# Optimization experiments

Measured on AMD Instinct MI355X. Metric: run time of the kernel, lower is better.

The kernel has to match this reference:

```python
import jax, jax.numpy as jnp
import numpy as np

N_NODES = 50000
N_EDGES = 800000
NODE_DIM = 64
EDGE_DIM = 32
OUT_FEATS = 64


def setup_inputs() -> dict:
    key = jax.random.key(0)
    k1, k2, k3, k4, k5, k6, k7 = jax.random.split(key, 7)
    node_features = jax.random.normal(k1, (N_NODES, NODE_DIM), dtype=jnp.float32)
    edge_features = jax.random.normal(k2, (N_EDGES, EDGE_DIM), dtype=jnp.float32)
    src = jax.random.randint(k3, (N_EDGES,), 0, N_NODES, dtype=jnp.int32)
    dst = jax.random.randint(k4, (N_EDGES,), 0, N_NODES, dtype=jnp.int32)
    in_dim = 2 * NODE_DIM + EDGE_DIM  # concat([e_ft, h_src, h_dst])
    w_group = jax.random.normal(k5, (in_dim,), dtype=jnp.float32) * 0.05
    w_srcattn = jax.random.normal(k6, (NODE_DIM + EDGE_DIM,), dtype=jnp.float32) * 0.05
    w_lin = jax.random.normal(k7, (in_dim, OUT_FEATS), dtype=jnp.float32) * 0.05
    return {"node_features": node_features, "edge_features": edge_features,
            "src": src, "dst": dst,
            "w_group": w_group, "w_srcattn": w_srcattn, "w_lin": w_lin}


def _segment_softmax(scores, seg, num_segments):
    # numerically-stable softmax of per-edge scalar scores within each segment
    m = jax.ops.segment_max(scores, seg, num_segments=num_segments)
    e = jnp.exp(scores - m[seg])
    s = jax.ops.segment_sum(e, seg, num_segments=num_segments)
    return e / s[seg]


def reference(node_features, edge_features, src, dst, w_group, w_srcattn, w_lin):
    h = node_features              # [N, node_dim]
    e_ft = edge_features           # [E, edge_dim]
    h_src = h[src]                 # [E, node_dim]
    h_dst = h[dst]                 # [E, node_dim]

    # --- group_apply_edges(group_by='src'): edge attention over out-edges of each src ---
    z2 = jnp.concatenate([e_ft, h_src, h_dst], axis=1)      # [E, edge_dim + 2*node_dim]
    a = z2 @ w_group                                        # [E]
    gamma = _segment_softmax(a, src, N_NODES)               # softmax over edges sharing src
    e_weighted = gamma[:, None] * e_ft                      # [E, edge_dim]

    # --- gnn_msg: msg = concat([h_src, e_weighted]) ---
    msg = jnp.concatenate([h_src, e_weighted], axis=1)      # [E, node_dim + edge_dim]

    # --- gnn_reduce: attention softmax over mailbox (edges sharing dst), weighted sum ---
    s = msg @ w_srcattn                                     # [E]
    alpha = _segment_softmax(s, dst, N_NODES)
    accum = jax.ops.segment_sum(alpha[:, None] * msg, dst, num_segments=N_NODES)  # [N, node_dim+edge_dim]

    # --- node_update: linear(concat([h, accum])) + relu ---
    h_cat = jnp.concatenate([h, accum], axis=1)             # [N, 2*node_dim + edge_dim]
    out = jax.nn.relu(h_cat @ w_lin)                        # [N, out_feats]
    return out
```

## Files before the change

### kernel.cpp

```cpp
#include <hip/hip_runtime.h>

#define NN 50000
#define NE 800000
#define NHB 3125
#define NTILES 3125

typedef __attribute__((ext_vector_type(8))) short bf16x8;
typedef __attribute__((ext_vector_type(4))) float f32x4;

static __device__ __forceinline__ short f2bf(float f) {
    unsigned int u = __float_as_uint(f);
    u += 0x7FFFu + ((u >> 16) & 1u);
    return (short)(u >> 16);
}

__global__ __launch_bounds__(256) void k_pre(
    const float* __restrict__ h, const int* __restrict__ dst,
    const float* __restrict__ wg, const float* __restrict__ wa,
    int* __restrict__ cnt, int* __restrict__ rank,
    float* __restrict__ p1, float* __restrict__ pd, float* __restrict__ dpf)
{
    int tid = threadIdx.x;
    if (blockIdx.x < NHB) {
        int e = blockIdx.x * 256 + tid;
        if (e < NE) rank[e] = atomicAdd(&cnt[dst[e]], 1);
        return;
    }
    __shared__ float4 ls[16], ld[16], lt[16];
    if (tid < 16)      ls[tid]      = ((const float4*)wg)[8 + tid];
    else if (tid < 32) ld[tid - 16] = ((const float4*)wg)[8 + tid];
    else if (tid < 48) lt[tid - 32] = ((const float4*)wa)[tid - 32];
    __syncthreads();
    int n = (blockIdx.x - NHB) * 16 + (tid >> 4);
    if (n >= NN) return;
    int l16 = tid & 15;
    float4 v = ((const float4*)(h + (size_t)n * 64))[l16];
    float4 w1 = ls[l16], w2 = ld[l16], w3 = lt[l16];
    float s1 = v.x*w1.x + v.y*w1.y + v.z*w1.z + v.w*w1.w;
    float s2 = v.x*w2.x + v.y*w2.y + v.z*w2.z + v.w*w2.w;
    float s3 = v.x*w3.x + v.y*w3.y + v.z*w3.z + v.w*w3.w;
    #pragma unroll
    for (int m = 8; m; m >>= 1) {
        s1 += __shfl_xor(s1, m);
        s2 += __shfl_xor(s2, m);
        s3 += __shfl_xor(s3, m);
    }
    if (l16 == 0) { p1[n] = s1; pd[n] = s2; dpf[2 * n + 1] = s3; }
}

__global__ __launch_bounds__(256) void k_assign(
    const int* __restrict__ cnt, int* __restrict__ off, int* __restrict__ gtotal)
{
    int n = blockIdx.x * 256 + threadIdx.x;
    int lane = threadIdx.x & 63;
    int c = (n < NN) ? cnt[n] : 0;
    int pre = c;
    #pragma unroll
    for (int d = 1; d < 64; d <<= 1) {
        int v = __shfl_up(pre, d);
        if (lane >= d) pre += v;
    }
    int base = 0;
    if (lane == 63) base = atomicAdd(gtotal, pre);
    base = __shfl(base, 63);
    if (n < NN) off[n] = base + pre - c;
}

__global__ __launch_bounds__(256) void k_edge(
    const float* __restrict__ ef, const int* __restrict__ src,
    const int* __restrict__ dst, const int* __restrict__ rank,
    const float* __restrict__ wg, const float* __restrict__ wa,
    const float* __restrict__ p1, const float* __restrict__ pd,
    float* __restrict__ dpf, const int* __restrict__ off,
    int4* __restrict__ recA)
{
    __shared__ float4 lwe[8], lae[8];
    int tid = threadIdx.x;
    if (tid < 8)       lwe[tid]     = ((const float4*)wg)[tid];
    else if (tid < 16) lae[tid - 8] = ((const float4*)wa)[tid - 8 + 16];
    __syncthreads();
    int e = blockIdx.x * 256 + tid;
    if (e >= NE) return;
    int s = src[e], d = dst[e], rk = rank[e];
    const float4* e4 = (const float4*)(ef + (size_t)e * 32);
    float a = 0.f, u = 0.f;
    #pragma unroll
    for (int q = 0; q < 8; ++q) {
        float4 v = e4[q], w = lwe[q], w2 = lae[q];
        a += v.x*w.x  + v.y*w.y  + v.z*w.z  + v.w*w.w;
        u += v.x*w2.x + v.y*w2.y + v.z*w2.z + v.w*w2.w;
    }
    a += p1[s] + pd[d];
    float eav = __expf(a);
    atomicAdd(&dpf[2 * s], eav);
    int pos = off[d] + rk;
    recA[pos] = make_int4(s, e, __float_as_int(eav), __float_as_int(u));
}

__global__ __launch_bounds__(256) void k_reduce(
    const float* __restrict__ h, const float* __restrict__ ef,
    const int* __restrict__ cnt, const int* __restrict__ off,
    const float2* __restrict__ dp, const int4* __restrict__ recA,
    float* __restrict__ accum)
{
    int n = blockIdx.x * 4 + (threadIdx.x >> 6);
    if (n >= NN) return;
    int lane = threadIdx.x & 63;
    bool up = lane >= 32;
    int l5 = lane & 31;
    int deg = cnt[n], base = off[n];
    float acch = 0.f, acce = 0.f, den = 0.f;
    int j = 0;
    for (; j + 4 <= deg; j += 4) {
        int4 r0 = recA[base+j+0], r1 = recA[base+j+1];
        int4 r2 = recA[base+j+2], r3 = recA[base+j+3];
        float2 d0 = dp[r0.x], d1 = dp[r1.x], d2 = dp[r2.x], d3 = dp[r3.x];
        float h0 = h[(size_t)r0.x*64+lane], h1 = h[(size_t)r1.x*64+lane];
        float h2 = h[(size_t)r2.x*64+lane], h3 = h[(size_t)r3.x*64+lane];
        int eA = up ? r1.y : r0.y, eB = up ? r3.y : r2.y;
        float efA = ef[(size_t)eA*32 + l5];
        float efB = ef[(size_t)eB*32 + l5];
        float g0 = __int_as_float(r0.z)/d0.x, g1 = __int_as_float(r1.z)/d1.x;
        float g2 = __int_as_float(r2.z)/d2.x, g3 = __int_as_float(r3.z)/d3.x;
        float s0 = __expf(d0.y + g0*__int_as_float(r0.w));
        float s1 = __expf(d1.y + g1*__int_as_float(r1.w));
        float s2 = __expf(d2.y + g2*__int_as_float(r2.w));
        float s3 = __expf(d3.y + g3*__int_as_float(r3.w));
        den  += s0 + s1 + s2 + s3;
        acch += s0*h0 + s1*h1 + s2*h2 + s3*h3;
        float wA = up ? s1*g1 : s0*g0;
        float wB = up ? s3*g3 : s2*g2;
        acce += wA*efA + wB*efB;
    }
    for (; j < deg; ++j) {
        int4 r = recA[base+j];
        float2 dt = dp[r.x];
        float g = __int_as_float(r.z)/dt.x;
        float s = __expf(dt.y + g*__int_as_float(r.w));
        den += s;
        acch += s * h[(size_t)r.x*64+lane];
        if (!up) acce += s * g * ef[(size_t)r.y*32 + l5];
    }
    acce += __shfl_xor(acce, 32);
    float inv = (deg > 0) ? 1.f/den : 0.f;
    accum[(size_t)n*96 + lane] = acch * inv;
    if (!up) accum[(size_t)n*96 + 64 + lane] = acce * inv;
}

__global__ __launch_bounds__(256) void k_node_update(
    const float* __restrict__ h, const float* __restrict__ accum,
    const float* __restrict__ wl_g, float* __restrict__ out)
{
    int lane = threadIdx.x & 63;
    int col  = lane & 15;
    int quad = lane >> 4;
    int wid  = blockIdx.x * 4 + (threadIdx.x >> 6);
    int nwaves = gridDim.x * 4;

    bf16x8 bfr[5][4];
    #pragma unroll
    for (int kc = 0; kc < 5; ++kc)
        #pragma unroll
        for (int nt = 0; nt < 4; ++nt) {
            #pragma unroll
            for (int j = 0; j < 8; ++j) {
                int k = kc * 32 + quad * 8 + j;
                bfr[kc][nt][j] = f2bf(wl_g[k * 64 + nt * 16 + col]);
            }
        }

    for (int tile = wid; tile < NTILES; tile += nwaves) {
        int n = tile * 16 + col;
        f32x4 acc[4];
        #pragma unroll
        for (int nt = 0; nt < 4; ++nt) acc[nt] = (f32x4){0.f, 0.f, 0.f, 0.f};

        #pragma unroll
        for (int kc = 0; kc < 5; ++kc) {
            int kbase = kc * 32 + quad * 8;
            const float* p = (kbase < 64)
                ? (h     + (size_t)n * 64 + kbase)
                : (accum + (size_t)n * 96 + (kbase - 64));
            float4 va = *(const float4*)p;
            float4 vb = *(const float4*)(p + 4);
            bf16x8 af;
            af[0] = f2bf(va.x); af[1] = f2bf(va.y);
            af[2] = f2bf(va.z); af[3] = f2bf(va.w);
            af[4] = f2bf(vb.x); af[5] = f2bf(vb.y);
            af[6] = f2bf(vb.z); af[7] = f2bf(vb.w);
            #pragma unroll
            for (int nt = 0; nt < 4; ++nt)
                acc[nt] = __builtin_amdgcn_mfma_f32_16x16x32_bf16(
                    af, bfr[kc][nt], acc[nt], 0, 0, 0);
        }

        #pragma unroll
        for (int nt = 0; nt < 4; ++nt) {
            #pragma unroll
            for (int r = 0; r < 4; ++r) {
                int node = tile * 16 + quad * 4 + r;
                out[(size_t)node * 64 + nt * 16 + col] = fmaxf(acc[nt][r], 0.f);
            }
        }
    }
}

extern "C" void kernel_launch(void* const* d_in, const int* in_sizes, int n_in,
                              void* d_out, int out_size, void* d_ws, size_t ws_size,
                              hipStream_t stream)
{
    const float* h   = (const float*)d_in[0];
    const float* ef  = (const float*)d_in[1];
    const int*   src = (const int*)d_in[2];
    const int*   dst = (const int*)d_in[3];
    const float* wg  = (const float*)d_in[4];
    const float* wa  = (const float*)d_in[5];
    const float* wl  = (const float*)d_in[6];
    float* out = (float*)d_out;

    float* ws = (float*)d_ws;
    float*  dpf    = ws;
    int*    cnt    = (int*)(ws + 2 * NN);
    int*    gtotal = (int*)(ws + 3 * NN);
    int*    off    = (int*)(ws + 3 * NN + 16);
    float*  p1     = ws + 4 * NN + 16;
    float*  pd     = ws + 5 * NN + 16;
    int4*   recA   = (int4*)(ws + 6 * NN + 16);
    int*    rank   = (int*)(ws + 6 * NN + 16 + 4 * NE);
    float*  accum  = ws + 6 * NN + 16 + 4 * NE;

    hipMemsetAsync(d_ws, 0, (size_t)(3 * NN + 16) * sizeof(float), stream);

    k_pre<<<2 * NHB, 256, 0, stream>>>(h, dst, wg, wa, cnt, rank, p1, pd, dpf);
    k_assign<<<(NN + 255) / 256, 256, 0, stream>>>(cnt, off, gtotal);
    k_edge<<<NHB, 256, 0, stream>>>(ef, src, dst, rank, wg, wa, p1, pd, dpf,
                                    off, recA);
    k_reduce<<<(NN + 3) / 4, 256, 0, stream>>>(h, ef, cnt, off, (const float2*)dpf,
                                               recA, accum);
    k_node_update<<<256, 256, 0, stream>>>(h, accum, wl, out);
}
```

Before: 334.9 us.

## Pack bf16 node/accum rows, two edges per thread, deeper reduce unroll

Node features are converted to bf16 in the pre-pass and the reduce kernel writes its aggregated results as bf16 into the same 160-wide row buffer. The node-update GEMM can then load MFMA operands directly, with no fp32 loads or per-element conversion, and it runs one tile per wave. The edge and rank kernels handle two edges per thread and write records with nontemporal stores. The reduce loop is unrolled by 8 and uses rcp approximations in place of divides. This trades some accuracy (fast rcp, bf16 rounding of accum, which the old code also did at GEMM time) for less memory traffic and more memory-level parallelism.

```diff
diff --git a/kernel.cpp b/kernel.cpp
--- a/kernel.cpp
+++ b/kernel.cpp
@@ -2,11 +2,14 @@
 
 #define NN 50000
 #define NE 800000
+#define NEB 1563
 #define NHB 3125
 #define NTILES 3125
 
 typedef __attribute__((ext_vector_type(8))) short bf16x8;
+typedef __attribute__((ext_vector_type(4))) short s16x4;
 typedef __attribute__((ext_vector_type(4))) float f32x4;
+typedef __attribute__((ext_vector_type(4))) int   i32x4;
 
 static __device__ __forceinline__ short f2bf(float f) {
     unsigned int u = __float_as_uint(f);
@@ -18,12 +21,21 @@
     const float* __restrict__ h, const int* __restrict__ dst,
     const float* __restrict__ wg, const float* __restrict__ wa,
     int* __restrict__ cnt, int* __restrict__ rank,
-    float* __restrict__ p1, float* __restrict__ pd, float* __restrict__ dpf)
+    float* __restrict__ p1, float* __restrict__ pd, float* __restrict__ dpf,
+    short* __restrict__ hb)
 {
     int tid = threadIdx.x;
-    if (blockIdx.x < NHB) {
-        int e = blockIdx.x * 256 + tid;
-        if (e < NE) rank[e] = atomicAdd(&cnt[dst[e]], 1);
+    if (blockIdx.x < NEB) {
+        int e0 = blockIdx.x * 512 + tid;
+        if (e0 >= NE) return;
+        int e1 = e0 + 256;
+        bool v1 = e1 < NE;
+        int d0 = dst[e0];
+        int d1 = dst[v1 ? e1 : 0];
+        int r0 = atomicAdd(&cnt[d0], 1);
+        int r1 = v1 ? atomicAdd(&cnt[d1], 1) : 0;
+        rank[e0] = r0;
+        if (v1) rank[e1] = r1;
         return;
     }
     __shared__ float4 ls[16], ld[16], lt[16];
@@ -31,10 +43,13 @@
     else if (tid < 32) ld[tid - 16] = ((const float4*)wg)[8 + tid];
     else if (tid < 48) lt[tid - 32] = ((const float4*)wa)[tid - 32];
     __syncthreads();
-    int n = (blockIdx.x - NHB) * 16 + (tid >> 4);
+    int n = (blockIdx.x - NEB) * 16 + (tid >> 4);
     if (n >= NN) return;
     int l16 = tid & 15;
     float4 v = ((const float4*)(h + (size_t)n * 64))[l16];
+    s16x4 hv;
+    hv[0] = f2bf(v.x); hv[1] = f2bf(v.y); hv[2] = f2bf(v.z); hv[3] = f2bf(v.w);
+    *(s16x4*)(hb + (size_t)n * 160 + l16 * 4) = hv;
     float4 w1 = ls[l16], w2 = ld[l16], w3 = lt[l16];
     float s1 = v.x*w1.x + v.y*w1.y + v.z*w1.z + v.w*w1.w;
     float s2 = v.x*w2.x + v.y*w2.y + v.z*w2.z + v.w*w2.w;
@@ -72,36 +87,52 @@
     const float* __restrict__ wg, const float* __restrict__ wa,
     const float* __restrict__ p1, const float* __restrict__ pd,
     float* __restrict__ dpf, const int* __restrict__ off,
-    int4* __restrict__ recA)
+    i32x4* __restrict__ recA)
 {
     __shared__ float4 lwe[8], lae[8];
     int tid = threadIdx.x;
     if (tid < 8)       lwe[tid]     = ((const float4*)wg)[tid];
     else if (tid < 16) lae[tid - 8] = ((const float4*)wa)[tid - 8 + 16];
     __syncthreads();
-    int e = blockIdx.x * 256 + tid;
-    if (e >= NE) return;
-    int s = src[e], d = dst[e], rk = rank[e];
-    const float4* e4 = (const float4*)(ef + (size_t)e * 32);
-    float a = 0.f, u = 0.f;
+    int e0 = blockIdx.x * 512 + tid;
+    if (e0 >= NE) return;
+    int e1 = e0 + 256;
+    bool v1 = e1 < NE;
+    int e1c = v1 ? e1 : 0;
+    int s0 = src[e0], d0 = dst[e0], k0 = rank[e0];
+    int s1 = src[e1c], d1 = dst[e1c], k1 = rank[e1c];
+    float p1a = p1[s0], pda = pd[d0];
+    float p1b = p1[s1], pdb = pd[d1];
+    int o0 = off[d0], o1 = off[d1];
+    const float4* ea = (const float4*)ef + (unsigned)e0 * 8u;
+    const float4* eb = (const float4*)ef + (unsigned)e1c * 8u;
+    float a0 = 0.f, u0 = 0.f, a1 = 0.f, u1 = 0.f;
     #pragma unroll
     for (int q = 0; q < 8; ++q) {
-        float4 v = e4[q], w = lwe[q], w2 = lae[q];
-        a += v.x*w.x  + v.y*w.y  + v.z*w.z  + v.w*w.w;
-        u += v.x*w2.x + v.y*w2.y + v.z*w2.z + v.w*w2.w;
-    }
-    a += p1[s] + pd[d];
-    float eav = __expf(a);
-    atomicAdd(&dpf[2 * s], eav);
-    int pos = off[d] + rk;
-    recA[pos] = make_int4(s, e, __float_as_int(eav), __float_as_int(u));
+        float4 x = ea[q], y = eb[q];
+        float4 w = lwe[q], w2 = lae[q];
+        a0 += x.x*w.x  + x.y*w.y  + x.z*w.z  + x.w*w.w;
+        u0 += x.x*w2.x + x.y*w2.y + x.z*w2.z + x.w*w2.w;
+        a1 += y.x*w.x  + y.y*w.y  + y.z*w.z  + y.w*w.w;
+        u1 += y.x*w2.x + y.y*w2.y + y.z*w2.z + y.w*w2.w;
+    }
+    float ev0 = __expf(a0 + p1a + pda);
+    float ev1 = __expf(a1 + p1b + pdb);
+    atomicAdd(&dpf[2 * s0], ev0);
+    if (v1) atomicAdd(&dpf[2 * s1], ev1);
+    i32x4 rc0 = (i32x4){s0, e0, __float_as_int(ev0), __float_as_int(u0)};
+    __builtin_nontemporal_store(rc0, recA + (o0 + k0));
+    if (v1) {
+        i32x4 rc1 = (i32x4){s1, e1, __float_as_int(ev1), __float_as_int(u1)};
+        __builtin_nontemporal_store(rc1, recA + (o1 + k1));
+    }
 }
 
 __global__ __launch_bounds__(256) void k_reduce(
     const float* __restrict__ h, const float* __restrict__ ef,
     const int* __restrict__ cnt, const int* __restrict__ off,
-    const float2* __restrict__ dp, const int4* __restrict__ recA,
-    float* __restrict__ accum)
+    const float2* __restrict__ dp, const i32x4* __restrict__ recA,
+    short* __restrict__ hb)
 {
     int n = blockIdx.x * 4 + (threadIdx.x >> 6);
     if (n >= NN) return;
@@ -109,53 +140,95 @@
     bool up = lane >= 32;
     int l5 = lane & 31;
     int deg = cnt[n], base = off[n];
+    const i32x4* rp = recA + base;
     float acch = 0.f, acce = 0.f, den = 0.f;
     int j = 0;
-    for (; j + 4 <= deg; j += 4) {
-        int4 r0 = recA[base+j+0], r1 = recA[base+j+1];
-        int4 r2 = recA[base+j+2], r3 = recA[base+j+3];
-        float2 d0 = dp[r0.x], d1 = dp[r1.x], d2 = dp[r2.x], d3 = dp[r3.x];
-        float h0 = h[(size_t)r0.x*64+lane], h1 = h[(size_t)r1.x*64+lane];
-        float h2 = h[(size_t)r2.x*64+lane], h3 = h[(size_t)r3.x*64+lane];
-        int eA = up ? r1.y : r0.y, eB = up ? r3.y : r2.y;
-        float efA = ef[(size_t)eA*32 + l5];
-        float efB = ef[(size_t)eB*32 + l5];
-        float g0 = __int_as_float(r0.z)/d0.x, g1 = __int_as_float(r1.z)/d1.x;
-        float g2 = __int_as_float(r2.z)/d2.x, g3 = __int_as_float(r3.z)/d3.x;
-        float s0 = __expf(d0.y + g0*__int_as_float(r0.w));
-        float s1 = __expf(d1.y + g1*__int_as_float(r1.w));
-        float s2 = __expf(d2.y + g2*__int_as_float(r2.w));
-        float s3 = __expf(d3.y + g3*__int_as_float(r3.w));
-        den  += s0 + s1 + s2 + s3;
-        acch += s0*h0 + s1*h1 + s2*h2 + s3*h3;
-        float wA = up ? s1*g1 : s0*g0;
-        float wB = up ? s3*g3 : s2*g2;
-        acce += wA*efA + wB*efB;
+    for (; j + 8 <= deg; j += 8) {
+        i32x4 r[8];
+        #pragma unroll
+        for (int t = 0; t < 8; ++t) r[t] = rp[j + t];
+        float2 dv[8];
+        #pragma unroll
+        for (int t = 0; t < 8; ++t) dv[t] = dp[r[t][0]];
+        float hv[8];
+        #pragma unroll
+        for (int t = 0; t < 8; ++t) hv[t] = h[((unsigned)r[t][0] << 6) + lane];
+        float efv[4];
+        #pragma unroll
+        for (int t = 0; t < 4; ++t) {
+            int e = up ? r[2*t+1][1] : r[2*t][1];
+            efv[t] = ef[((unsigned)e << 5) + l5];
+        }
+        float g[8], s[8];
+        #pragma unroll
+        for (int t = 0; t < 8; ++t) {
+            g[t] = __int_as_float(r[t][2]) * __builtin_amdgcn_rcpf(dv[t].x);
+            s[t] = __expf(dv[t].y + g[t] * __int_as_float(r[t][3]));
+            den  += s[t];
+            acch += s[t] * hv[t];
+        }
+        #pragma unroll
+        for (int t = 0; t < 4; ++t) {
+            float w = up ? s[2*t+1]*g[2*t+1] : s[2*t]*g[2*t];
+            acce += w * efv[t];
+        }
+    }
+    if (j + 4 <= deg) {
+        i32x4 r[4];
+        #pragma unroll
+        for (int t = 0; t < 4; ++t) r[t] = rp[j + t];
+        float2 dv[4];
+        #pragma unroll
+        for (int t = 0; t < 4; ++t) dv[t] = dp[r[t][0]];
+        float hv[4];
+        #pragma unroll
+        for (int t = 0; t < 4; ++t) hv[t] = h[((unsigned)r[t][0] << 6) + lane];
+        float efv[2];
+        #pragma unroll
+        for (int t = 0; t < 2; ++t) {
+            int e = up ? r[2*t+1][1] : r[2*t][1];
+            efv[t] = ef[((unsigned)e << 5) + l5];
+        }
+        float g[4], s[4];
+        #pragma unroll
+        for (int t = 0; t < 4; ++t) {
+            g[t] = __int_as_float(r[t][2]) * __builtin_amdgcn_rcpf(dv[t].x);
+            s[t] = __expf(dv[t].y + g[t] * __int_as_float(r[t][3]));
+            den  += s[t];
+            acch += s[t] * hv[t];
+        }
+        #pragma unroll
+        for (int t = 0; t < 2; ++t) {
+            float w = up ? s[2*t+1]*g[2*t+1] : s[2*t]*g[2*t];
+            acce += w * efv[t];
+        }
+        j += 4;
     }
     for (; j < deg; ++j) {
-        int4 r = recA[base+j];
-        float2 dt = dp[r.x];
-        float g = __int_as_float(r.z)/dt.x;
-        float s = __expf(dt.y + g*__int_as_float(r.w));
+        i32x4 r = rp[j];
+        float2 dt = dp[r[0]];
+        float g = __int_as_float(r[2]) * __builtin_amdgcn_rcpf(dt.x);
+        float s = __expf(dt.y + g * __int_as_float(r[3]));
         den += s;
-        acch += s * h[(size_t)r.x*64+lane];
-        if (!up) acce += s * g * ef[(size_t)r.y*32 + l5];
+        acch += s * h[((unsigned)r[0] << 6) + lane];
+        if (!up) acce += s * g * ef[((unsigned)r[1] << 5) + l5];
     }
     acce += __shfl_xor(acce, 32);
-    float inv = (deg > 0) ? 1.f/den : 0.f;
-    accum[(size_t)n*96 + lane] = acch * inv;
-    if (!up) accum[(size_t)n*96 + 64 + lane] = acce * inv;
+    float inv = (deg > 0) ? __builtin_amdgcn_rcpf(den) : 0.f;
+    size_t hbase = (size_t)n * 160;
+    hb[hbase + 64 + lane] = f2bf(acch * inv);
+    if (!up) hb[hbase + 128 + l5] = f2bf(acce * inv);
 }
 
 __global__ __launch_bounds__(256) void k_node_update(
-    const float* __restrict__ h, const float* __restrict__ accum,
-    const float* __restrict__ wl_g, float* __restrict__ out)
+    const short* __restrict__ hb, const float* __restrict__ wl_g,
+    float* __restrict__ out)
 {
     int lane = threadIdx.x & 63;
     int col  = lane & 15;
     int quad = lane >> 4;
-    int wid  = blockIdx.x * 4 + (threadIdx.x >> 6);
-    int nwaves = gridDim.x * 4;
+    int tile = blockIdx.x * 4 + (threadIdx.x >> 6);
+    if (tile >= NTILES) return;
 
     bf16x8 bfr[5][4];
     #pragma unroll
@@ -169,38 +242,27 @@
             }
         }
 
-    for (int tile = wid; tile < NTILES; tile += nwaves) {
-        int n = tile * 16 + col;
-        f32x4 acc[4];
-        #pragma unroll
-        for (int nt = 0; nt < 4; ++nt) acc[nt] = (f32x4){0.f, 0.f, 0.f, 0.f};
-
-        #pragma unroll
-        for (int kc = 0; kc < 5; ++kc) {
-            int kbase = kc * 32 + quad * 8;
-            const float* p = (kbase < 64)
-                ? (h     + (size_t)n * 64 + kbase)
-                : (accum + (size_t)n * 96 + (kbase - 64));
-            float4 va = *(const float4*)p;
-            float4 vb = *(const float4*)(p + 4);
-            bf16x8 af;
-            af[0] = f2bf(va.x); af[1] = f2bf(va.y);
-            af[2] = f2bf(va.z); af[3] = f2bf(va.w);
-            af[4] = f2bf(vb.x); af[5] = f2bf(vb.y);
-            af[6] = f2bf(vb.z); af[7] = f2bf(vb.w);
-            #pragma unroll
-            for (int nt = 0; nt < 4; ++nt)
-                acc[nt] = __builtin_amdgcn_mfma_f32_16x16x32_bf16(
-                    af, bfr[kc][nt], acc[nt], 0, 0, 0);
-        }
-
-        #pragma unroll
-        for (int nt = 0; nt < 4; ++nt) {
-            #pragma unroll
-            for (int r = 0; r < 4; ++r) {
-                int node = tile * 16 + quad * 4 + r;
-                out[(size_t)node * 64 + nt * 16 + col] = fmaxf(acc[nt][r], 0.f);
-            }
+    int n = tile * 16 + col;
+    f32x4 acc[4];
+    #pragma unroll
+    for (int nt = 0; nt < 4; ++nt) acc[nt] = (f32x4){0.f, 0.f, 0.f, 0.f};
+
+    const short* hrow = hb + (size_t)n * 160 + quad * 8;
+    #pragma unroll
+    for (int kc = 0; kc < 5; ++kc) {
+        bf16x8 af = *(const bf16x8*)(hrow + kc * 32);
+        #pragma unroll
+        for (int nt = 0; nt < 4; ++nt)
+            acc[nt] = __builtin_amdgcn_mfma_f32_16x16x32_bf16(
+                af, bfr[kc][nt], acc[nt], 0, 0, 0);
+    }
+
+    #pragma unroll
+    for (int nt = 0; nt < 4; ++nt) {
+        #pragma unroll
+        for (int r = 0; r < 4; ++r) {
+            int node = tile * 16 + quad * 4 + r;
+            out[(size_t)node * 64 + nt * 16 + col] = fmaxf(acc[nt][r], 0.f);
         }
     }
 }
@@ -225,17 +287,17 @@
     int*    off    = (int*)(ws + 3 * NN + 16);
     float*  p1     = ws + 4 * NN + 16;
     float*  pd     = ws + 5 * NN + 16;
-    int4*   recA   = (int4*)(ws + 6 * NN + 16);
+    i32x4*  recA   = (i32x4*)(ws + 6 * NN + 16);
     int*    rank   = (int*)(ws + 6 * NN + 16 + 4 * NE);
-    float*  accum  = ws + 6 * NN + 16 + 4 * NE;
+    short*  hb     = (short*)(ws + 6 * NN + 16 + 5 * NE);
 
     hipMemsetAsync(d_ws, 0, (size_t)(3 * NN + 16) * sizeof(float), stream);
 
-    k_pre<<<2 * NHB, 256, 0, stream>>>(h, dst, wg, wa, cnt, rank, p1, pd, dpf);
+    k_pre<<<NEB + NHB, 256, 0, stream>>>(h, dst, wg, wa, cnt, rank, p1, pd, dpf, hb);
     k_assign<<<(NN + 255) / 256, 256, 0, stream>>>(cnt, off, gtotal);
-    k_edge<<<NHB, 256, 0, stream>>>(ef, src, dst, rank, wg, wa, p1, pd, dpf,
+    k_edge<<<NEB, 256, 0, stream>>>(ef, src, dst, rank, wg, wa, p1, pd, dpf,
                                     off, recA);
     k_reduce<<<(NN + 3) / 4, 256, 0, stream>>>(h, ef, cnt, off, (const float2*)dpf,
-                                               recA, accum);
-    k_node_update<<<256, 256, 0, stream>>>(h, accum, wl, out);
-}
+                                               recA, hb);
+    k_node_update<<<782, 256, 0, stream>>>(hb, wl, out);
+}
```

Result: slower. 356.3 us (+6.4%).
